# Kernel tuning notes

Measured on AMD Instinct MI355X. Metric: run time of the kernel, lower is better.

Reference implementation:

```python
import jax, jax.numpy as jnp
import numpy as np

N, E, D, H, L, G, C = 50000, 800000, 128, 128, 3, 128, 10
BN_EPS = 1e-5


def setup_inputs() -> dict:
    key = jax.random.key(0)
    ks = jax.random.split(key, 16)
    inp = {
        "x": jax.random.normal(ks[0], (N, D), dtype=jnp.float32),
        "node_centrality": jax.random.uniform(ks[1], (N,), dtype=jnp.float32),
        "edge_centrality": jax.random.uniform(ks[2], (E,), dtype=jnp.float32),
        # stacked per-layer MLP params (in == hidden so stackable)
        "W1": jax.random.normal(ks[3], (L, D, H), dtype=jnp.float32) * 0.05,
        "b1": jnp.zeros((L, H), dtype=jnp.float32),
        "g1": jnp.ones((L, H), dtype=jnp.float32),
        "be1": jnp.zeros((L, H), dtype=jnp.float32),
        "W2": jax.random.normal(ks[4], (L, H, H), dtype=jnp.float32) * 0.05,
        "b2": jnp.zeros((L, H), dtype=jnp.float32),
        "Wc": jax.random.normal(ks[5], (H, C), dtype=jnp.float32) * 0.05,
        "bc": jnp.zeros((C,), dtype=jnp.float32),
        "edge_index": jax.random.randint(ks[6], (2, E), 0, N, dtype=jnp.int64),
        "batch": jnp.sort(jax.random.randint(ks[7], (N,), 0, G, dtype=jnp.int64)),
    }
    return inp


def _gin_forward(x, node_centrality, edge_centrality, W1, b1, g1, be1, W2, b2, Wc, bc, edge_index, batch):
    src, dst = edge_index[0], edge_index[1]  # x_j = x[src], aggregate at dst
    ec = edge_centrality[:, None]
    nc = node_centrality[:, None]
    for l in range(L):
        # message: gather + scale by edge centrality; aggr='add': scatter-add
        msg = x[src] * ec                                      # [E, H]
        agg = jax.ops.segment_sum(msg, dst, num_segments=N)    # [N, H]
        h = agg * nc + x                                       # (1 + eps) * x_r, eps = 0
        # MLP([in, hidden, hidden]): Linear -> BatchNorm(train) -> ReLU -> Linear
        h = h @ W1[l] + b1[l]
        mu = h.mean(axis=0)
        var = h.var(axis=0)  # biased, matches BN training stats
        h = (h - mu) * jax.lax.rsqrt(var + BN_EPS) * g1[l] + be1[l]
        h = jax.nn.relu(h)
        h = h @ W2[l] + b2[l]
        x = jax.nn.relu(h)  # outer .relu() in GIN.forward
    # global mean pool over graphs
    sums = jax.ops.segment_sum(x, batch, num_segments=G)           # [G, H]
    cnt = jax.ops.segment_sum(jnp.ones((N,), x.dtype), batch, num_segments=G)
    pooled = sums / jnp.maximum(cnt, 1.0)[:, None]
    return pooled @ Wc + bc  # [G, C]


def reference(x, edge_index, batch, node_centrality, edge_centrality, W1, b1, g1, be1, W2, b2, Wc, bc):
    return _gin_forward(x, node_centrality, edge_centrality, W1, b1, g1, be1, W2, b2, Wc, bc, edge_index, batch)
```

## Files before the change

kernel.cpp:

```cpp
#include <hip/hip_runtime.h>
#include <hip/hip_fp16.h>

#define Nn 50000
#define Ee 800000
#define HD 128
#define Ll 3
#define Gg 128
#define Cc 10
#define BN_EPS 1e-5f
#define NBLK1 782
#define NPART 1564
#define PPAD 1600
#define NSCB 49

typedef __attribute__((ext_vector_type(8))) __bf16 bf16x8;
typedef __attribute__((ext_vector_type(4))) __bf16 bf16x4;
typedef __attribute__((ext_vector_type(4))) float f32x4;

__global__ void k_deg(const int* __restrict__ dst, int* __restrict__ deg) {
  int i = blockIdx.x * blockDim.x + threadIdx.x;
  int base = i * 4;
  if (base >= Ee) return;
#pragma unroll
  for (int j = 0; j < 4; ++j) {
    int e = base + j;
    if (e < Ee) atomicAdd(&deg[dst[e]], 1);
  }
}

__global__ void k_scan1(const int* __restrict__ deg, int* __restrict__ offs,
                        int* __restrict__ bsum) {
  __shared__ int b0[1024], b1[1024];
  int tid = threadIdx.x;
  int i = blockIdx.x * 1024 + tid;
  int v = (i < Nn) ? deg[i] : 0;
  int* cur = b0; int* nxt = b1;
  cur[tid] = v;
  __syncthreads();
  for (int off = 1; off < 1024; off <<= 1) {
    int s = cur[tid] + ((tid >= off) ? cur[tid - off] : 0);
    nxt[tid] = s;
    __syncthreads();
    int* t = cur; cur = nxt; nxt = t;
  }
  if (i < Nn) offs[i] = cur[tid] - v;
  if (tid == 1023) bsum[blockIdx.x] = cur[1023];
}

__global__ void k_scan2(const int* __restrict__ bsum, int* __restrict__ carry) {
  int lane = threadIdx.x;
  int v = (lane < NSCB) ? bsum[lane] : 0;
  int s = v;
  for (int off = 1; off < 64; off <<= 1) {
    int t = __shfl_up(s, off, 64);
    if (lane >= off) s += t;
  }
  if (lane < NSCB) carry[lane] = s - v;
}

__global__ void k_scan3(const int* __restrict__ carry, int* __restrict__ offs,
                        int* __restrict__ cursor) {
  int i = blockIdx.x * 1024 + threadIdx.x;
  if (i < Nn) {
    int o = offs[i] + carry[blockIdx.x];
    offs[i] = o; cursor[i] = o;
  }
  if (i == 0) offs[Nn] = Ee;
}

__global__ void k_fill(const int* __restrict__ src, const int* __restrict__ dst,
                       const float* __restrict__ ec, int* __restrict__ cursor,
                       unsigned int* __restrict__ epk) {
  int i = blockIdx.x * blockDim.x + threadIdx.x;
  int base = i * 4;
  if (base >= Ee) return;
  int d[4], s[4], p[4]; unsigned short hb[4]; bool ok[4];
#pragma unroll
  for (int j = 0; j < 4; ++j) {
    int e = base + j;
    ok[j] = e < Ee;
    if (ok[j]) {
      d[j] = dst[e]; s[j] = src[e];
      hb[j] = __half_as_ushort(__float2half(ec[e]));
    }
  }
#pragma unroll
  for (int j = 0; j < 4; ++j)
    if (ok[j]) p[j] = atomicAdd(&cursor[d[j]], 1);
#pragma unroll
  for (int j = 0; j < 4; ++j)
    if (ok[j]) epk[p[j]] = ((unsigned int)s[j] << 16) | hb[j];
}

__global__ void k_xcast(const float* __restrict__ x, __bf16* __restrict__ xb) {
  int i = blockIdx.x * blockDim.x + threadIdx.x;
  int stride = gridDim.x * blockDim.x;
  const int n4 = Nn * 32;
  for (int t = i; t < n4; t += stride) {
    f32x4 v = ((const f32x4*)x)[t];
    bf16x4 b;
#pragma unroll
    for (int j = 0; j < 4; ++j) b[j] = (__bf16)v[j];
    ((bf16x4*)xb)[t] = b;
  }
}

__global__ void k_wprep(const float* __restrict__ W1, const float* __restrict__ W2,
                        __bf16* __restrict__ wtHi, __bf16* __restrict__ wtLo) {
  int mat = blockIdx.x >> 3;
  int chunk = blockIdx.x & 7;
  const float* W = (mat < 3) ? (W1 + mat * 16384) : (W2 + (mat - 3) * 16384);
  __bf16* hi = wtHi + mat * 16384;
  __bf16* lo = wtLo + mat * 16384;
  for (int t = threadIdx.x; t < 2048; t += blockDim.x) {
    int idx = chunk * 2048 + t;
    int n = idx >> 7, k = idx & 127;
    float v = W[k * 128 + n];
    __bf16 h = (__bf16)v;
    hi[idx] = h;
    lo[idx] = (__bf16)(v - (float)h);
  }
}

__global__ void k_agg(const __bf16* __restrict__ xb, const int* __restrict__ offs,
                      const unsigned int* __restrict__ epk, float* __restrict__ agg) {
  int wid = threadIdx.x >> 6, lane = threadIdx.x & 63;
  int n = blockIdx.x * 4 + wid;
  if (n >= Nn) return;
  int beg = offs[n], end = offs[n + 1];
  const unsigned int* x2 = (const unsigned int*)xb;
  float ax0 = 0.f, ay0 = 0.f, ax1 = 0.f, ay1 = 0.f;
  float ax2 = 0.f, ay2 = 0.f, ax3 = 0.f, ay3 = 0.f;
  int j = beg;
  for (; j + 3 < end; j += 4) {
    unsigned int e0 = epk[j], e1 = epk[j + 1], e2 = epk[j + 2], e3 = epk[j + 3];
    unsigned int v0 = x2[(e0 >> 16) * 64 + lane];
    unsigned int v1 = x2[(e1 >> 16) * 64 + lane];
    unsigned int v2 = x2[(e2 >> 16) * 64 + lane];
    unsigned int v3 = x2[(e3 >> 16) * 64 + lane];
    __half_raw h0, h1, h2, h3;
    h0.x = (unsigned short)(e0 & 0xffffu); h1.x = (unsigned short)(e1 & 0xffffu);
    h2.x = (unsigned short)(e2 & 0xffffu); h3.x = (unsigned short)(e3 & 0xffffu);
    float w0 = __half2float(h0), w1 = __half2float(h1);
    float w2 = __half2float(h2), w3 = __half2float(h3);
    ax0 = fmaf(__uint_as_float(v0 << 16), w0, ax0);
    ay0 = fmaf(__uint_as_float(v0 & 0xffff0000u), w0, ay0);
    ax1 = fmaf(__uint_as_float(v1 << 16), w1, ax1);
    ay1 = fmaf(__uint_as_float(v1 & 0xffff0000u), w1, ay1);
    ax2 = fmaf(__uint_as_float(v2 << 16), w2, ax2);
    ay2 = fmaf(__uint_as_float(v2 & 0xffff0000u), w2, ay2);
    ax3 = fmaf(__uint_as_float(v3 << 16), w3, ax3);
    ay3 = fmaf(__uint_as_float(v3 & 0xffff0000u), w3, ay3);
  }
  for (; j < end; ++j) {
    unsigned int e = epk[j];
    unsigned int v = x2[(e >> 16) * 64 + lane];
    __half_raw h; h.x = (unsigned short)(e & 0xffffu);
    float w = __half2float(h);
    ax0 = fmaf(__uint_as_float(v << 16), w, ax0);
    ay0 = fmaf(__uint_as_float(v & 0xffff0000u), w, ay0);
  }
  float2 acc = make_float2(ax0 + ax1 + ax2 + ax3, ay0 + ay1 + ay2 + ay3);
  ((float2*)agg)[n * 64 + lane] = acc;
}

__device__ __forceinline__ void split8(const float* a, bf16x8& hi, bf16x8& lo) {
#pragma unroll
  for (int j = 0; j < 8; ++j) {
    float v = a[j];
    __bf16 h = (__bf16)v;
    hi[j] = h;
    lo[j] = (__bf16)(v - (float)h);
  }
}

__launch_bounds__(256)
__global__ void k_gemm1(const float* __restrict__ agg, const float* __restrict__ nc,
                        const __bf16* __restrict__ xb,
                        const __bf16* __restrict__ wtHi, const __bf16* __restrict__ wtLo,
                        const float* __restrict__ bias, float* __restrict__ out,
                        float* __restrict__ partial) {
  int tid = threadIdx.x;
  int w = tid >> 6, l = tid & 63;
  int wr = w >> 1, wc = w & 1;
  int row0 = blockIdx.x * 64 + wr * 32;
  int l15 = l & 15, lg = l >> 4;
  int colw = wc * 64;
  int krow = lg * 8;

  f32x4 acc[2][4];
#pragma unroll
  for (int m = 0; m < 2; ++m)
#pragma unroll
    for (int n = 0; n < 4; ++n) acc[m][n] = (f32x4){0.f, 0.f, 0.f, 0.f};

  int rowA[2]; bool rv[2]; float ncv[2];
#pragma unroll
  for (int m = 0; m < 2; ++m) {
    rowA[m] = row0 + m * 16 + l15;
    rv[m] = rowA[m] < Nn;
    ncv[m] = rv[m] ? nc[rowA[m]] : 0.f;
  }

#pragma unroll
  for (int ks = 0; ks < 4; ++ks) {
    int k0 = ks * 32 + krow;
    bf16x8 aHi[2], aLo[2];
#pragma unroll
    for (int m = 0; m < 2; ++m) {
      float av[8];
      if (rv[m]) {
        const float* ap = agg + rowA[m] * 128 + k0;
        bf16x8 xv = *(const bf16x8*)(xb + rowA[m] * 128 + k0);
        f32x4 g0 = *(const f32x4*)ap, g1 = *(const f32x4*)(ap + 4);
#pragma unroll
        for (int jj = 0; jj < 4; ++jj) {
          av[jj]     = fmaf(g0[jj], ncv[m], (float)xv[jj]);
          av[4 + jj] = fmaf(g1[jj], ncv[m], (float)xv[4 + jj]);
        }
      } else {
#pragma unroll
        for (int jj = 0; jj < 8; ++jj) av[jj] = 0.f;
      }
      split8(av, aHi[m], aLo[m]);
    }
    bf16x8 bHi[4], bLo[4];
#pragma unroll
    for (int n = 0; n < 4; ++n) {
      int c = colw + n * 16 + l15;
      bHi[n] = *(const bf16x8*)(wtHi + c * 128 + k0);
      bLo[n] = *(const bf16x8*)(wtLo + c * 128 + k0);
    }
#pragma unroll
    for (int m = 0; m < 2; ++m)
#pragma unroll
      for (int n = 0; n < 4; ++n) {
        acc[m][n] = __builtin_amdgcn_mfma_f32_16x16x32_bf16(aHi[m], bHi[n], acc[m][n], 0, 0, 0);
        acc[m][n] = __builtin_amdgcn_mfma_f32_16x16x32_bf16(aLo[m], bHi[n], acc[m][n], 0, 0, 0);
        acc[m][n] = __builtin_amdgcn_mfma_f32_16x16x32_bf16(aHi[m], bLo[n], acc[m][n], 0, 0, 0);
      }
  }

  float s[4] = {0.f, 0.f, 0.f, 0.f}, q[4] = {0.f, 0.f, 0.f, 0.f};
#pragma unroll
  for (int n = 0; n < 4; ++n) {
    int c = colw + n * 16 + l15;
    float bv = bias[c];
#pragma unroll
    for (int m = 0; m < 2; ++m) {
      int rbase = row0 + m * 16 + lg * 4;
#pragma unroll
      for (int r = 0; r < 4; ++r) {
        int rr = rbase + r;
        if (rr < Nn) {
          float o = acc[m][n][r] + bv;
          out[rr * 128 + c] = o;
          s[n] += o; q[n] += o * o;
        }
      }
    }
  }
#pragma unroll
  for (int n = 0; n < 4; ++n) {
    s[n] += __shfl_xor(s[n], 16, 64); q[n] += __shfl_xor(q[n], 16, 64);
    s[n] += __shfl_xor(s[n], 32, 64); q[n] += __shfl_xor(q[n], 32, 64);
  }
  if (lg == 0) {
    int slot = blockIdx.x * 2 + wr;
#pragma unroll
    for (int n = 0; n < 4; ++n) {
      int f = colw + n * 16 + l15;
      partial[f * PPAD + slot] = s[n];
      partial[(128 + f) * PPAD + slot] = q[n];
    }
  }
}

__global__ void k_bnfin(const float* __restrict__ partial,
                        const float* __restrict__ g1, const float* __restrict__ be1,
                        float* __restrict__ scaleA, float* __restrict__ shiftA) {
  __shared__ float ss[256], qq[256];
  int f = blockIdx.x, t = threadIdx.x;
  float s = 0.f, q = 0.f;
  for (int b = t; b < NPART; b += 256) {
    s += partial[f * PPAD + b];
    q += partial[(128 + f) * PPAD + b];
  }
  ss[t] = s; qq[t] = q;
  __syncthreads();
  for (int off = 128; off > 0; off >>= 1) {
    if (t < off) { ss[t] += ss[t + off]; qq[t] += qq[t + off]; }
    __syncthreads();
  }
  if (t == 0) {
    const float inv = 1.0f / (float)Nn;
    float mu = ss[0] * inv;
    float var = fmaxf(qq[0] * inv - mu * mu, 0.f);
    float rs = rsqrtf(var + BN_EPS);
    float sc = rs * g1[f];
    scaleA[f] = sc;
    shiftA[f] = be1[f] - mu * sc;
  }
}

__launch_bounds__(256)
__global__ void k_gemm2(const float* __restrict__ h1, const float* __restrict__ scaleA,
                        const float* __restrict__ shiftA,
                        const __bf16* __restrict__ wtHi, const __bf16* __restrict__ wtLo,
                        const float* __restrict__ bias, __bf16* __restrict__ xbout) {
  int tid = threadIdx.x;
  int w = tid >> 6, l = tid & 63;
  int wr = w >> 1, wc = w & 1;
  int row0 = blockIdx.x * 64 + wr * 32;
  int l15 = l & 15, lg = l >> 4;
  int colw = wc * 64;
  int krow = lg * 8;

  f32x4 acc[2][4];
#pragma unroll
  for (int m = 0; m < 2; ++m)
#pragma unroll
    for (int n = 0; n < 4; ++n) acc[m][n] = (f32x4){0.f, 0.f, 0.f, 0.f};

  int rowA[2]; bool rv[2];
#pragma unroll
  for (int m = 0; m < 2; ++m) {
    rowA[m] = row0 + m * 16 + l15;
    rv[m] = rowA[m] < Nn;
  }

#pragma unroll
  for (int ks = 0; ks < 4; ++ks) {
    int k0 = ks * 32 + krow;
    f32x4 sc0 = *(const f32x4*)(scaleA + k0), sc1 = *(const f32x4*)(scaleA + k0 + 4);
    f32x4 sh0 = *(const f32x4*)(shiftA + k0), sh1 = *(const f32x4*)(shiftA + k0 + 4);
    bf16x8 aHi[2], aLo[2];
#pragma unroll
    for (int m = 0; m < 2; ++m) {
      float av[8];
      if (rv[m]) {
        const float* hp = h1 + rowA[m] * 128 + k0;
        f32x4 h0 = *(const f32x4*)hp, h1v = *(const f32x4*)(hp + 4);
#pragma unroll
        for (int jj = 0; jj < 4; ++jj) {
          av[jj]     = fmaxf(fmaf(h0[jj],  sc0[jj], sh0[jj]), 0.f);
          av[4 + jj] = fmaxf(fmaf(h1v[jj], sc1[jj], sh1[jj]), 0.f);
        }
      } else {
#pragma unroll
        for (int jj = 0; jj < 8; ++jj) av[jj] = 0.f;
      }
      split8(av, aHi[m], aLo[m]);
    }
    bf16x8 bHi[4], bLo[4];
#pragma unroll
    for (int n = 0; n < 4; ++n) {
      int c = colw + n * 16 + l15;
      bHi[n] = *(const bf16x8*)(wtHi + c * 128 + k0);
      bLo[n] = *(const bf16x8*)(wtLo + c * 128 + k0);
    }
#pragma unroll
    for (int m = 0; m < 2; ++m)
#pragma unroll
      for (int n = 0; n < 4; ++n) {
        acc[m][n] = __builtin_amdgcn_mfma_f32_16x16x32_bf16(aHi[m], bHi[n], acc[m][n], 0, 0, 0);
        acc[m][n] = __builtin_amdgcn_mfma_f32_16x16x32_bf16(aLo[m], bHi[n], acc[m][n], 0, 0, 0);
        acc[m][n] = __builtin_amdgcn_mfma_f32_16x16x32_bf16(aHi[m], bLo[n], acc[m][n], 0, 0, 0);
      }
  }

#pragma unroll
  for (int n = 0; n < 4; ++n) {
    int c = colw + n * 16 + l15;
    float bv = bias[c];
#pragma unroll
    for (int m = 0; m < 2; ++m) {
      int rbase = row0 + m * 16 + lg * 4;
#pragma unroll
      for (int r = 0; r < 4; ++r) {
        int rr = rbase + r;
        if (rr < Nn) xbout[rr * 128 + c] = (__bf16)fmaxf(acc[m][n][r] + bv, 0.f);
      }
    }
  }
}

#define PCH 64
__global__ void k_pool(const __bf16* __restrict__ xb, const int* __restrict__ batch,
                       float* __restrict__ pooled, float* __restrict__ gcnt) {
  int wid = threadIdx.x >> 6, lane = threadIdx.x & 63;
  int w = blockIdx.x * 4 + wid;
  int n0 = w * PCH;
  if (n0 >= Nn) return;
  int n1 = (n0 + PCH < Nn) ? n0 + PCH : Nn;
  const unsigned int* x2 = (const unsigned int*)xb;
  float2 acc = make_float2(0.f, 0.f);
  int cur = batch[n0];
  int cnt = 0;
  for (int n = n0; n < n1; ++n) {
    int g = batch[n];
    if (g != cur) {
      atomicAdd(&pooled[cur * 128 + lane * 2 + 0], acc.x);
      atomicAdd(&pooled[cur * 128 + lane * 2 + 1], acc.y);
      if (lane == 0) atomicAdd(&gcnt[cur], (float)cnt);
      acc = make_float2(0.f, 0.f); cnt = 0; cur = g;
    }
    unsigned int v = x2[n * 64 + lane];
    acc.x += __uint_as_float(v << 16);
    acc.y += __uint_as_float(v & 0xffff0000u);
    ++cnt;
  }
  atomicAdd(&pooled[cur * 128 + lane * 2 + 0], acc.x);
  atomicAdd(&pooled[cur * 128 + lane * 2 + 1], acc.y);
  if (lane == 0) atomicAdd(&gcnt[cur], (float)cnt);
}

__global__ void k_head(const float* __restrict__ pooled, const float* __restrict__ gcnt,
                       const float* __restrict__ Wc, const float* __restrict__ bc,
                       float* __restrict__ out) {
  __shared__ float p[128];
  int g = blockIdx.x, tid = threadIdx.x;
  p[tid] = pooled[g * 128 + tid] / fmaxf(gcnt[g], 1.0f);
  __syncthreads();
  if (tid < Cc) {
    float acc = bc[tid];
    for (int k = 0; k < 128; ++k) acc = fmaf(p[k], Wc[k * Cc + tid], acc);
    out[g * Cc + tid] = acc;
  }
}

extern "C" void kernel_launch(void* const* d_in, const int* in_sizes, int n_in,
                              void* d_out, int out_size, void* d_ws, size_t ws_size,
                              hipStream_t stream) {
  const float* x    = (const float*)d_in[0];
  const float* ncn  = (const float*)d_in[1];
  const float* ecn  = (const float*)d_in[2];
  const float* W1   = (const float*)d_in[3];
  const float* b1   = (const float*)d_in[4];
  const float* g1   = (const float*)d_in[5];
  const float* be1  = (const float*)d_in[6];
  const float* W2   = (const float*)d_in[7];
  const float* b2   = (const float*)d_in[8];
  const float* Wc   = (const float*)d_in[9];
  const float* bc   = (const float*)d_in[10];
  const int*   ei   = (const int*)d_in[11];
  const int*   batch= (const int*)d_in[12];
  const int* src  = ei;
  const int* dstp = ei + Ee;

  float* fws = (float*)d_ws;
  float* agg      = fws;
  float* h1       = fws +  6400000;
  float* partial  = fws + 12800000;
  float* scaleA   = partial + 256 * PPAD;
  float* shiftA   = scaleA + 128;
  float* pooled   = shiftA + 128;
  float* gcnt     = pooled + Gg * 128;
  int*   deg      = (int*)(gcnt + 128);
  int*   offs     = deg + Nn;
  int*   cursor   = offs + Nn + 64;
  int*   bsum     = cursor + Nn;
  int*   carry    = bsum + 64;
  unsigned int* epk = (unsigned int*)(carry + 64);
  __bf16* wtHi    = (__bf16*)(epk + Ee);
  __bf16* wtLo    = wtHi + 6 * 16384;
  __bf16* xb      = wtLo + 6 * 16384;

  k_wprep<<<48, 256, 0, stream>>>(W1, W2, wtHi, wtLo);
  k_xcast<<<2048, 256, 0, stream>>>(x, xb);
  hipMemsetAsync(deg, 0, Nn * sizeof(int), stream);
  k_deg<<<(Ee / 4 + 255) / 256, 256, 0, stream>>>(dstp, deg);
  k_scan1<<<NSCB, 1024, 0, stream>>>(deg, offs, bsum);
  k_scan2<<<1, 64, 0, stream>>>(bsum, carry);
  k_scan3<<<NSCB, 1024, 0, stream>>>(carry, offs, cursor);
  k_fill<<<(Ee / 4 + 255) / 256, 256, 0, stream>>>(src, dstp, ecn, cursor, epk);

  for (int l = 0; l < Ll; ++l) {
    k_agg<<<(Nn + 3) / 4, 256, 0, stream>>>(xb, offs, epk, agg);
    k_gemm1<<<NBLK1, 256, 0, stream>>>(agg, ncn, xb,
                                       wtHi + l * 16384, wtLo + l * 16384,
                                       b1 + l * 128, h1, partial);
    k_bnfin<<<128, 256, 0, stream>>>(partial, g1 + l * 128, be1 + l * 128,
                                     scaleA, shiftA);
    k_gemm2<<<NBLK1, 256, 0, stream>>>(h1, scaleA, shiftA,
                                       wtHi + (3 + l) * 16384, wtLo + (3 + l) * 16384,
                                       b2 + l * 128, xb);
  }

  hipMemsetAsync(pooled, 0, (Gg * 128 + 128) * sizeof(float), stream);
  k_pool<<<(Nn + PCH * 4 - 1) / (PCH * 4), 256, 0, stream>>>(xb, batch, pooled, gcnt);
  k_head<<<Gg, 128, 0, stream>>>(pooled, gcnt, Wc, bc, (float*)d_out);
}
```

Before: 553.3 us.

## Store agg and h1 intermediates in bf16, unroll gather by 8

The aggregation output and the first GEMM output are now stored as bf16 instead of fp32, which halves the global traffic of writing and re-reading these N×128 intermediates in every layer. The aggregation loop is unrolled to 8 independent gathers with 8 accumulator pairs, giving more loads in flight. The CSR fill now uses nontemporal stores. BN statistics are still computed from fp32 values, but GEMM2 reads the bf16-rounded h1, so accuracy drops slightly.

```diff
diff --git a/kernel.cpp b/kernel.cpp
--- a/kernel.cpp
+++ b/kernel.cpp
@@ -15,6 +15,7 @@
 
 typedef __attribute__((ext_vector_type(8))) __bf16 bf16x8;
 typedef __attribute__((ext_vector_type(4))) __bf16 bf16x4;
+typedef __attribute__((ext_vector_type(2))) __bf16 bf16x2;
 typedef __attribute__((ext_vector_type(4))) float f32x4;
 
 __global__ void k_deg(const int* __restrict__ dst, int* __restrict__ deg) {
@@ -89,7 +90,8 @@
     if (ok[j]) p[j] = atomicAdd(&cursor[d[j]], 1);
 #pragma unroll
   for (int j = 0; j < 4; ++j)
-    if (ok[j]) epk[p[j]] = ((unsigned int)s[j] << 16) | hb[j];
+    if (ok[j]) __builtin_nontemporal_store(((unsigned int)s[j] << 16) | hb[j],
+                                           &epk[p[j]]);
 }
 
 __global__ void k_xcast(const float* __restrict__ x, __bf16* __restrict__ xb) {
@@ -123,45 +125,42 @@
 }
 
 __global__ void k_agg(const __bf16* __restrict__ xb, const int* __restrict__ offs,
-                      const unsigned int* __restrict__ epk, float* __restrict__ agg) {
+                      const unsigned int* __restrict__ epk, __bf16* __restrict__ aggb) {
   int wid = threadIdx.x >> 6, lane = threadIdx.x & 63;
   int n = blockIdx.x * 4 + wid;
   if (n >= Nn) return;
   int beg = offs[n], end = offs[n + 1];
   const unsigned int* x2 = (const unsigned int*)xb;
-  float ax0 = 0.f, ay0 = 0.f, ax1 = 0.f, ay1 = 0.f;
-  float ax2 = 0.f, ay2 = 0.f, ax3 = 0.f, ay3 = 0.f;
+  float ax[8], ay[8];
+#pragma unroll
+  for (int t = 0; t < 8; ++t) { ax[t] = 0.f; ay[t] = 0.f; }
   int j = beg;
-  for (; j + 3 < end; j += 4) {
-    unsigned int e0 = epk[j], e1 = epk[j + 1], e2 = epk[j + 2], e3 = epk[j + 3];
-    unsigned int v0 = x2[(e0 >> 16) * 64 + lane];
-    unsigned int v1 = x2[(e1 >> 16) * 64 + lane];
-    unsigned int v2 = x2[(e2 >> 16) * 64 + lane];
-    unsigned int v3 = x2[(e3 >> 16) * 64 + lane];
-    __half_raw h0, h1, h2, h3;
-    h0.x = (unsigned short)(e0 & 0xffffu); h1.x = (unsigned short)(e1 & 0xffffu);
-    h2.x = (unsigned short)(e2 & 0xffffu); h3.x = (unsigned short)(e3 & 0xffffu);
-    float w0 = __half2float(h0), w1 = __half2float(h1);
-    float w2 = __half2float(h2), w3 = __half2float(h3);
-    ax0 = fmaf(__uint_as_float(v0 << 16), w0, ax0);
-    ay0 = fmaf(__uint_as_float(v0 & 0xffff0000u), w0, ay0);
-    ax1 = fmaf(__uint_as_float(v1 << 16), w1, ax1);
-    ay1 = fmaf(__uint_as_float(v1 & 0xffff0000u), w1, ay1);
-    ax2 = fmaf(__uint_as_float(v2 << 16), w2, ax2);
-    ay2 = fmaf(__uint_as_float(v2 & 0xffff0000u), w2, ay2);
-    ax3 = fmaf(__uint_as_float(v3 << 16), w3, ax3);
-    ay3 = fmaf(__uint_as_float(v3 & 0xffff0000u), w3, ay3);
+  for (; j + 7 < end; j += 8) {
+    unsigned int e[8], v[8];
+#pragma unroll
+    for (int t = 0; t < 8; ++t) e[t] = epk[j + t];
+#pragma unroll
+    for (int t = 0; t < 8; ++t) v[t] = x2[(e[t] >> 16) * 64 + lane];
+#pragma unroll
+    for (int t = 0; t < 8; ++t) {
+      __half_raw h; h.x = (unsigned short)(e[t] & 0xffffu);
+      float w = __half2float(h);
+      ax[t] = fmaf(__uint_as_float(v[t] << 16), w, ax[t]);
+      ay[t] = fmaf(__uint_as_float(v[t] & 0xffff0000u), w, ay[t]);
+    }
   }
   for (; j < end; ++j) {
     unsigned int e = epk[j];
     unsigned int v = x2[(e >> 16) * 64 + lane];
     __half_raw h; h.x = (unsigned short)(e & 0xffffu);
     float w = __half2float(h);
-    ax0 = fmaf(__uint_as_float(v << 16), w, ax0);
-    ay0 = fmaf(__uint_as_float(v & 0xffff0000u), w, ay0);
-  }
-  float2 acc = make_float2(ax0 + ax1 + ax2 + ax3, ay0 + ay1 + ay2 + ay3);
-  ((float2*)agg)[n * 64 + lane] = acc;
+    ax[0] = fmaf(__uint_as_float(v << 16), w, ax[0]);
+    ay[0] = fmaf(__uint_as_float(v & 0xffff0000u), w, ay[0]);
+  }
+  float sx = (ax[0] + ax[1]) + (ax[2] + ax[3]) + ((ax[4] + ax[5]) + (ax[6] + ax[7]));
+  float sy = (ay[0] + ay[1]) + (ay[2] + ay[3]) + ((ay[4] + ay[5]) + (ay[6] + ay[7]));
+  bf16x2 o; o[0] = (__bf16)sx; o[1] = (__bf16)sy;
+  ((bf16x2*)aggb)[n * 64 + lane] = o;
 }
 
 __device__ __forceinline__ void split8(const float* a, bf16x8& hi, bf16x8& lo) {
@@ -175,10 +174,10 @@
 }
 
 __launch_bounds__(256)
-__global__ void k_gemm1(const float* __restrict__ agg, const float* __restrict__ nc,
+__global__ void k_gemm1(const __bf16* __restrict__ aggb, const float* __restrict__ nc,
                         const __bf16* __restrict__ xb,
                         const __bf16* __restrict__ wtHi, const __bf16* __restrict__ wtLo,
-                        const float* __restrict__ bias, float* __restrict__ out,
+                        const float* __restrict__ bias, __bf16* __restrict__ h1b,
                         float* __restrict__ partial) {
   int tid = threadIdx.x;
   int w = tid >> 6, l = tid & 63;
@@ -210,14 +209,11 @@
     for (int m = 0; m < 2; ++m) {
       float av[8];
       if (rv[m]) {
-        const float* ap = agg + rowA[m] * 128 + k0;
+        bf16x8 ag = *(const bf16x8*)(aggb + rowA[m] * 128 + k0);
         bf16x8 xv = *(const bf16x8*)(xb + rowA[m] * 128 + k0);
-        f32x4 g0 = *(const f32x4*)ap, g1 = *(const f32x4*)(ap + 4);
-#pragma unroll
-        for (int jj = 0; jj < 4; ++jj) {
-          av[jj]     = fmaf(g0[jj], ncv[m], (float)xv[jj]);
-          av[4 + jj] = fmaf(g1[jj], ncv[m], (float)xv[4 + jj]);
-        }
+#pragma unroll
+        for (int jj = 0; jj < 8; ++jj)
+          av[jj] = fmaf((float)ag[jj], ncv[m], (float)xv[jj]);
       } else {
 #pragma unroll
         for (int jj = 0; jj < 8; ++jj) av[jj] = 0.f;
@@ -254,7 +250,7 @@
         int rr = rbase + r;
         if (rr < Nn) {
           float o = acc[m][n][r] + bv;
-          out[rr * 128 + c] = o;
+          h1b[rr * 128 + c] = (__bf16)o;
           s[n] += o; q[n] += o * o;
         }
       }
@@ -304,7 +300,7 @@
 }
 
 __launch_bounds__(256)
-__global__ void k_gemm2(const float* __restrict__ h1, const float* __restrict__ scaleA,
+__global__ void k_gemm2(const __bf16* __restrict__ h1b, const float* __restrict__ scaleA,
                         const float* __restrict__ shiftA,
                         const __bf16* __restrict__ wtHi, const __bf16* __restrict__ wtLo,
                         const float* __restrict__ bias, __bf16* __restrict__ xbout) {
@@ -339,12 +335,11 @@
     for (int m = 0; m < 2; ++m) {
       float av[8];
       if (rv[m]) {
-        const float* hp = h1 + rowA[m] * 128 + k0;
-        f32x4 h0 = *(const f32x4*)hp, h1v = *(const f32x4*)(hp + 4);
+        bf16x8 hv = *(const bf16x8*)(h1b + rowA[m] * 128 + k0);
 #pragma unroll
         for (int jj = 0; jj < 4; ++jj) {
-          av[jj]     = fmaxf(fmaf(h0[jj],  sc0[jj], sh0[jj]), 0.f);
-          av[4 + jj] = fmaxf(fmaf(h1v[jj], sc1[jj], sh1[jj]), 0.f);
+          av[jj]     = fmaxf(fmaf((float)hv[jj],     sc0[jj], sh0[jj]), 0.f);
+          av[4 + jj] = fmaxf(fmaf((float)hv[4 + jj], sc1[jj], sh1[jj]), 0.f);
         }
       } else {
 #pragma unroll
@@ -449,9 +444,7 @@
   const int* dstp = ei + Ee;
 
   float* fws = (float*)d_ws;
-  float* agg      = fws;
-  float* h1       = fws +  6400000;
-  float* partial  = fws + 12800000;
+  float* partial  = fws;
   float* scaleA   = partial + 256 * PPAD;
   float* shiftA   = scaleA + 128;
   float* pooled   = shiftA + 128;
@@ -465,6 +458,8 @@
   __bf16* wtHi    = (__bf16*)(epk + Ee);
   __bf16* wtLo    = wtHi + 6 * 16384;
   __bf16* xb      = wtLo + 6 * 16384;
+  __bf16* aggb    = xb + Nn * 128;
+  __bf16* h1b     = aggb + Nn * 128;
 
   k_wprep<<<48, 256, 0, stream>>>(W1, W2, wtHi, wtLo);
   k_xcast<<<2048, 256, 0, stream>>>(x, xb);
@@ -476,13 +471,13 @@
   k_fill<<<(Ee / 4 + 255) / 256, 256, 0, stream>>>(src, dstp, ecn, cursor, epk);
 
   for (int l = 0; l < Ll; ++l) {
-    k_agg<<<(Nn + 3) / 4, 256, 0, stream>>>(xb, offs, epk, agg);
-    k_gemm1<<<NBLK1, 256, 0, stream>>>(agg, ncn, xb,
+    k_agg<<<(Nn + 3) / 4, 256, 0, stream>>>(xb, offs, epk, aggb);
+    k_gemm1<<<NBLK1, 256, 0, stream>>>(aggb, ncn, xb,
                                        wtHi + l * 16384, wtLo + l * 16384,
-                                       b1 + l * 128, h1, partial);
+                                       b1 + l * 128, h1b, partial);
     k_bnfin<<<128, 256, 0, stream>>>(partial, g1 + l * 128, be1 + l * 128,
                                      scaleA, shiftA);
-    k_gemm2<<<NBLK1, 256, 0, stream>>>(h1, scaleA, shiftA,
+    k_gemm2<<<NBLK1, 256, 0, stream>>>(h1b, scaleA, shiftA,
                                        wtHi + (3 + l) * 16384, wtLo + (3 + l) * 16384,
                                        b2 + l * 128, xb);
   }
```

After: 545.3 us. About the same (-1.4%).
